# Kernel optimization log

Measured on AMD Instinct MI355X. Metric: run time of the kernel, lower is better.

## Reference

```python
import jax, jax.numpy as jnp
import numpy as np


def _topk_gate(v, k):
    # keep values >= k-th largest (ties kept, matching torch semantics)
    topk_vals = jax.lax.top_k(v, k)[0]          # (B, k)
    thr = topk_vals[:, -1:]                      # (B, 1)
    return v * (v >= thr).astype(v.dtype)


def setup_inputs() -> dict:
    key = jax.random.key(0)
    ks = jax.random.split(key, 12)
    B, S, D, R, M = 8, 2048, 1024, 64, 256
    H = 4 * D
    def lin(k, fan_out, fan_in):
        bound = 1.0 / np.sqrt(fan_in)
        return jax.random.uniform(k, (fan_out, fan_in), jnp.float32, -bound, bound)
    def bias(k, fan_out, fan_in):
        bound = 1.0 / np.sqrt(fan_in)
        return jax.random.uniform(k, (fan_out,), jnp.float32, -bound, bound)
    return {
        "x": jax.random.normal(ks[0], (B, S, D), jnp.float32),
        "state": jnp.zeros((B, M), jnp.float32),
        "U_w": lin(ks[1], R, D),
        "V_w": lin(ks[2], R, D),
        "w1": lin(ks[3], H, D),
        "b1": bias(ks[4], H, D),
        "w2": lin(ks[5], D, H),
        "b2": bias(ks[6], D, H),
        "win_w": lin(ks[7], M, D),
        "win_b": bias(ks[8], M, D),
        "wstate": lin(ks[9], M, M),
        "gamma": jnp.float32(0.9),
        "top_k": 32,
    }


def reference(x, state, U_w, V_w, w1, b1, w2, b2, win_w, win_b, wstate, gamma, top_k):
    # outputs depend only on x (residual + FFN), computed vectorized over seq.
    h = jax.nn.relu(jnp.einsum("bsd,hd->bsh", x, w1) + b1)
    outputs = x + jnp.einsum("bsh,dh->bsd", h, w2) + b2   # (B, S, D)
    # Note: U_proj / V_proj are computed but unused in the original forward
    # (dead code); omitted here as they do not affect outputs or memory.

    # precompute W_in projection for all timesteps: (B, S, M)
    x_proj = jnp.einsum("bsd,md->bsm", x, win_w) + win_b

    def step(carry, xp_t):
        st, mem = carry
        su = jax.nn.relu(st @ wstate.T + xp_t)            # (B, M)
        g = _topk_gate(su, top_k)
        mem = gamma * mem + (1.0 - gamma) * g
        return (g, mem), None

    (_, memory), _ = jax.lax.scan(step, (state, state), jnp.swapaxes(x_proj, 0, 1))
    return outputs, memory
```

## Files before the change

### kernel.cpp

```cpp
#include <hip/hip_runtime.h>
#include <stdint.h>

#define BB 8
#define SS 2048
#define DD 1024
#define HH 4096
#define MM 256

typedef short bf16x8 __attribute__((ext_vector_type(8)));
typedef float f32x4 __attribute__((ext_vector_type(4)));

__device__ inline unsigned short f2bf(float f){
  unsigned u = __builtin_bit_cast(unsigned, f);
  return (unsigned short)((u + 0x7FFFu + ((u >> 16) & 1u)) >> 16);
}

__global__ void ssma_pack_bf16(const float* __restrict__ src,
                               unsigned short* __restrict__ dst, int n4){
  int i = blockIdx.x * blockDim.x + threadIdx.x;
  if (i < n4){
    float4 v = ((const float4*)src)[i];
    ushort4 o;
    o.x = f2bf(v.x); o.y = f2bf(v.y); o.z = f2bf(v.z); o.w = f2bf(v.w);
    ((ushort4*)dst)[i] = o;
  }
}

template<int EPI>
__global__ __launch_bounds__(256) void ssma_gemm_bt(
    const unsigned short* __restrict__ A, const unsigned short* __restrict__ Bw,
    int K, int N, const float* __restrict__ bias,
    const float* __restrict__ resid, void* __restrict__ Cout)
{
  __shared__ uint4 As4[512];
  __shared__ uint4 Bs4[512];
  unsigned short* As = (unsigned short*)As4;
  unsigned short* Bs = (unsigned short*)Bs4;

  const int tid  = threadIdx.x;
  const int lane = tid & 63;
  const int wv   = tid >> 6;
  const int wm   = wv >> 1, wn = wv & 1;
  const int m0   = blockIdx.y * 128;
  const int n0   = blockIdx.x * 128;
  const int kq   = lane >> 4;
  const int rl   = lane & 15;

  f32x4 acc[4][4];
#pragma unroll
  for (int a = 0; a < 4; ++a)
#pragma unroll
    for (int b = 0; b < 4; ++b) acc[a][b] = (f32x4){0.f, 0.f, 0.f, 0.f};

  for (int k0 = 0; k0 < K; k0 += 32){
    __syncthreads();
#pragma unroll
    for (int i = 0; i < 2; ++i){
      int c  = tid + 256 * i;
      int r  = c >> 2;
      int c8 = (c & 3) * 8;
      As4[c] = *(const uint4*)(A  + (size_t)(m0 + r) * K + k0 + c8);
      Bs4[c] = *(const uint4*)(Bw + (size_t)(n0 + r) * K + k0 + c8);
    }
    __syncthreads();

    const bf16x8* Ap = (const bf16x8*)As;
    const bf16x8* Bp = (const bf16x8*)Bs;
    bf16x8 af[4], bfr[4];
#pragma unroll
    for (int mi = 0; mi < 4; ++mi) af[mi]  = Ap[(wm * 64 + mi * 16 + rl) * 4 + kq];
#pragma unroll
    for (int ni = 0; ni < 4; ++ni) bfr[ni] = Bp[(wn * 64 + ni * 16 + rl) * 4 + kq];
#pragma unroll
    for (int mi = 0; mi < 4; ++mi)
#pragma unroll
      for (int ni = 0; ni < 4; ++ni)
        acc[mi][ni] = __builtin_amdgcn_mfma_f32_16x16x32_bf16(af[mi], bfr[ni], acc[mi][ni], 0, 0, 0);
  }

#pragma unroll
  for (int mi = 0; mi < 4; ++mi){
#pragma unroll
    for (int ni = 0; ni < 4; ++ni){
      int col = n0 + wn * 64 + ni * 16 + rl;
      float bv = bias[col];
#pragma unroll
      for (int r = 0; r < 4; ++r){
        int row = m0 + wm * 64 + mi * 16 + kq * 4 + r;
        float v = acc[mi][ni][r] + bv;
        if (EPI == 0){
          v = fmaxf(v, 0.0f);
          ((unsigned short*)Cout)[(size_t)row * N + col] = f2bf(v);
        } else {
          v += resid[(size_t)row * N + col];
          ((float*)Cout)[(size_t)row * N + col] = v;
        }
      }
    }
  }
}

__global__ __launch_bounds__(256) void ssma_gemm3_f32(
    const float* __restrict__ A, const float* __restrict__ Bw,
    const float* __restrict__ bias, float* __restrict__ C)
{
  __shared__ float As[64][17];
  __shared__ float Bs[64][17];
  const int tid = threadIdx.x;
  const int tx = tid & 15, ty = tid >> 4;
  const int m0 = blockIdx.y * 64, n0 = blockIdx.x * 64;
  float acc[4][4];
#pragma unroll
  for (int i = 0; i < 4; ++i)
#pragma unroll
    for (int j = 0; j < 4; ++j) acc[i][j] = 0.f;

  for (int k0 = 0; k0 < DD; k0 += 16){
    __syncthreads();
#pragma unroll
    for (int i = 0; i < 4; ++i){
      int e = tid + 256 * i;
      int r = e >> 4, c = e & 15;
      As[r][c] = A [(size_t)(m0 + r) * DD + k0 + c];
      Bs[r][c] = Bw[(size_t)(n0 + r) * DD + k0 + c];
    }
    __syncthreads();
#pragma unroll
    for (int kk = 0; kk < 16; ++kk){
      float a[4], b[4];
#pragma unroll
      for (int i = 0; i < 4; ++i) a[i] = As[ty * 4 + i][kk];
#pragma unroll
      for (int j = 0; j < 4; ++j) b[j] = Bs[tx * 4 + j][kk];
#pragma unroll
      for (int i = 0; i < 4; ++i)
#pragma unroll
        for (int j = 0; j < 4; ++j) acc[i][j] = fmaf(a[i], b[j], acc[i][j]);
    }
  }
#pragma unroll
  for (int i = 0; i < 4; ++i){
    int row = m0 + ty * 4 + i;
#pragma unroll
    for (int j = 0; j < 4; ++j){
      int col = n0 + tx * 4 + j;
      C[(size_t)row * MM + col] = acc[i][j] + bias[col];
    }
  }
}

__global__ __launch_bounds__(256) void ssma_transpose(
    const float* __restrict__ A, float* __restrict__ At)
{
  __shared__ float t[32][33];
  const int tx = threadIdx.x & 31, ty = threadIdx.x >> 5;
  const int x0 = blockIdx.x * 32, y0 = blockIdx.y * 32;
#pragma unroll
  for (int r = 0; r < 32; r += 8)
    t[ty + r][tx] = A[(size_t)(y0 + ty + r) * MM + x0 + tx];
  __syncthreads();
#pragma unroll
  for (int r = 0; r < 32; r += 8)
    At[(size_t)(x0 + ty + r) * MM + y0 + tx] = t[tx][ty + r];
}

__global__ __launch_bounds__(1024, 4) void ssma_scan5(
    const float* __restrict__ xproj, const float* __restrict__ state,
    const float* __restrict__ wT, const float* __restrict__ gamma_p,
    const int* __restrict__ topk_p, float* __restrict__ mem_out)
{
  __shared__ __align__(16) float su_all[MM];
  __shared__ __align__(16) int   kidx[MM + 32];
  __shared__ __align__(16) float kval[MM + 32];
  __shared__ __align__(16) unsigned long long umask[4];
  __shared__ __align__(16) int   kmask16[16];

  const int tid  = threadIdx.x;
  const int wv   = tid >> 6;
  const int lane = tid & 63;
  const int b    = blockIdx.x;
  const float gamma = *gamma_p;
  const float omg   = 1.0f - gamma;
  const int   rk    = *topk_p - 1;

  const int r = tid >> 2;
  const int q = tid & 3;

  const float* xp  = xproj + (size_t)b * SS * MM;
  const float* wTm = wT + tid;

  float mem = state[b * MM + r];

  float st0 = 0.0f;
  if (tid < MM){
    st0 = state[b * MM + tid];
    unsigned long long pmi = __ballot(st0 != 0.0f);
    if (lane == 0) umask[wv] = pmi;
  }
  __syncthreads();
  int nkp;
  {
    unsigned long long u0 = umask[0], u1 = umask[1], u2 = umask[2], u3 = umask[3];
    int nk = __popcll(u0) + __popcll(u1) + __popcll(u2) + __popcll(u3);
    if (tid < MM && st0 != 0.0f){
      int before = (wv > 0 ? __popcll(u0) : 0) + (wv > 1 ? __popcll(u1) : 0)
                 + (wv > 2 ? __popcll(u2) : 0);
      unsigned long long mw = (wv == 0 ? u0 : wv == 1 ? u1 : wv == 2 ? u2 : u3);
      int pos = before + __popcll(mw & ((1ull << lane) - 1ull));
      kidx[pos] = tid << 8;
      kval[pos] = st0;
    }
    nkp = (nk + 15) & ~15; if (nkp < 32) nkp = 32;
    if (tid >= MM && tid < MM + 64){
      int t2 = tid - MM;
      if (nk + t2 < nkp){ kidx[nk + t2] = 0; kval[nk + t2] = 0.0f; }
    }
  }
  float xp_cur = (tid < MM) ? xp[tid] : 0.0f;
  __syncthreads();

  for (int t = 0; t < SS; ++t){
    float xp_next = 0.0f;
    if (tid < MM){
      int tn = (t + 1 < SS) ? t + 1 : SS - 1;
      xp_next = xp[(size_t)tn * MM + tid];

      const int4*   ip = (const int4*)kidx;
      const float4* vp = (const float4*)kval;
      int4   I[8];
      float4 V[8];
#pragma unroll
      for (int j = 0; j < 8; ++j){ I[j] = ip[j]; V[j] = vp[j]; }
      float a0=0.f,a1=0.f,a2=0.f,a3=0.f,a4=0.f,a5=0.f,a6=0.f,a7=0.f;
      float w00=wTm[I[0].x], w01=wTm[I[0].y], w02=wTm[I[0].z], w03=wTm[I[0].w];
      float w10=wTm[I[1].x], w11=wTm[I[1].y], w12=wTm[I[1].z], w13=wTm[I[1].w];
      float w20=wTm[I[2].x], w21=wTm[I[2].y], w22=wTm[I[2].z], w23=wTm[I[2].w];
      float w30=wTm[I[3].x], w31=wTm[I[3].y], w32=wTm[I[3].z], w33=wTm[I[3].w];
      float w40=wTm[I[4].x], w41=wTm[I[4].y], w42=wTm[I[4].z], w43=wTm[I[4].w];
      float w50=wTm[I[5].x], w51=wTm[I[5].y], w52=wTm[I[5].z], w53=wTm[I[5].w];
      float w60=wTm[I[6].x], w61=wTm[I[6].y], w62=wTm[I[6].z], w63=wTm[I[6].w];
      float w70=wTm[I[7].x], w71=wTm[I[7].y], w72=wTm[I[7].z], w73=wTm[I[7].w];
      a0=fmaf(w00,V[0].x,a0); a0=fmaf(w01,V[0].y,a0); a0=fmaf(w02,V[0].z,a0); a0=fmaf(w03,V[0].w,a0);
      a1=fmaf(w10,V[1].x,a1); a1=fmaf(w11,V[1].y,a1); a1=fmaf(w12,V[1].z,a1); a1=fmaf(w13,V[1].w,a1);
      a2=fmaf(w20,V[2].x,a2); a2=fmaf(w21,V[2].y,a2); a2=fmaf(w22,V[2].z,a2); a2=fmaf(w23,V[2].w,a2);
      a3=fmaf(w30,V[3].x,a3); a3=fmaf(w31,V[3].y,a3); a3=fmaf(w32,V[3].z,a3); a3=fmaf(w33,V[3].w,a3);
      a4=fmaf(w40,V[4].x,a4); a4=fmaf(w41,V[4].y,a4); a4=fmaf(w42,V[4].z,a4); a4=fmaf(w43,V[4].w,a4);
      a5=fmaf(w50,V[5].x,a5); a5=fmaf(w51,V[5].y,a5); a5=fmaf(w52,V[5].z,a5); a5=fmaf(w53,V[5].w,a5);
      a6=fmaf(w60,V[6].x,a6); a6=fmaf(w61,V[6].y,a6); a6=fmaf(w62,V[6].z,a6); a6=fmaf(w63,V[6].w,a6);
      a7=fmaf(w70,V[7].x,a7); a7=fmaf(w71,V[7].y,a7); a7=fmaf(w72,V[7].z,a7); a7=fmaf(w73,V[7].w,a7);
      if (nkp > 32){
        for (int c4 = 8; c4 < (nkp >> 2); ++c4){
          int4 I2 = ip[c4]; float4 V2 = vp[c4];
          a0 = fmaf(wTm[I2.x], V2.x, a0); a1 = fmaf(wTm[I2.y], V2.y, a1);
          a2 = fmaf(wTm[I2.z], V2.z, a2); a3 = fmaf(wTm[I2.w], V2.w, a3);
        }
      }
      float s = ((a0 + a1) + (a2 + a3)) + ((a4 + a5) + (a6 + a7));
      su_all[tid] = fmaxf(s + xp_cur, 0.0f);
    }
    __syncthreads();

    float su2 = su_all[r];
    int cnt = 0;
    const float4* spp = (const float4*)su_all;
#pragma unroll
    for (int i = 0; i < 16; ++i){
      float4 v = spp[i * 4 + q];
      cnt += (v.x > su2) + (v.y > su2) + (v.z > su2) + (v.w > su2);
    }
    cnt += __shfl_xor(cnt, 1);
    cnt += __shfl_xor(cnt, 2);

    float g = (su2 > 0.0f && cnt <= rk) ? su2 : 0.0f;
    if (q == 0) mem = fmaf(gamma, mem, omg * g);

    unsigned long long kb = __ballot(q == 0 && g > 0.0f);
    unsigned long long kbS = kb & 0x1111111111111111ull;
    if (lane == 0) kmask16[wv] = __popcll(kbS);
    __syncthreads();

    {
      int4 k0 = *(const int4*)&kmask16[0];
      int4 k1 = *(const int4*)&kmask16[4];
      int4 k2 = *(const int4*)&kmask16[8];
      int4 k3 = *(const int4*)&kmask16[12];
      int cw[16] = {k0.x,k0.y,k0.z,k0.w, k1.x,k1.y,k1.z,k1.w,
                    k2.x,k2.y,k2.z,k2.w, k3.x,k3.y,k3.z,k3.w};
      int nk = 0, before = 0;
#pragma unroll
      for (int w = 0; w < 16; ++w){
        nk += cw[w];
        if (w < wv) before += cw[w];
      }
      if (q == 0 && g > 0.0f){
        int pos = before + __popcll(kbS & ((1ull << lane) - 1ull));
        kidx[pos] = r << 8;
        kval[pos] = g;
      }
      nkp = (nk + 15) & ~15; if (nkp < 32) nkp = 32;
      if (tid < 64){
        if (nk + tid < nkp){ kidx[nk + tid] = 0; kval[nk + tid] = 0.0f; }
      }
    }
    xp_cur = xp_next;
    __syncthreads();
  }
  if (q == 0) mem_out[b * MM + r] = mem;
}

extern "C" void kernel_launch(void* const* d_in, const int* in_sizes, int n_in,
                              void* d_out, int out_size, void* d_ws, size_t ws_size,
                              hipStream_t stream)
{
  const float* x      = (const float*)d_in[0];
  const float* state  = (const float*)d_in[1];
  const float* w1     = (const float*)d_in[4];
  const float* b1     = (const float*)d_in[5];
  const float* w2     = (const float*)d_in[6];
  const float* b2     = (const float*)d_in[7];
  const float* win_w  = (const float*)d_in[8];
  const float* win_b  = (const float*)d_in[9];
  const float* wstate = (const float*)d_in[10];
  const float* gammap = (const float*)d_in[11];
  const int*   topkp  = (const int*)d_in[12];

  float* out  = (float*)d_out;
  float* memo = out + (size_t)BB * SS * DD;

  char* ws = (char*)d_ws;
  unsigned short* xb   = (unsigned short*)(ws);
  unsigned short* w1b  = (unsigned short*)(ws + 33554432);
  unsigned short* w2b  = (unsigned short*)(ws + 41943040);
  unsigned short* hbuf = (unsigned short*)(ws + 50331648);
  float*          xprj = (float*)(ws + 184549376);
  float*          wT   = (float*)(ws + 33554432);

  ssma_pack_bf16<<<16384, 256, 0, stream>>>(x,  xb,  4194304);
  ssma_pack_bf16<<<4096,  256, 0, stream>>>(w1, w1b, 1048576);
  ssma_pack_bf16<<<4096,  256, 0, stream>>>(w2, w2b, 1048576);

  ssma_gemm3_f32<<<dim3(4, 256), 256, 0, stream>>>(x, win_w, win_b, xprj);

  ssma_gemm_bt<0><<<dim3(32, 128), 256, 0, stream>>>(xb, w1b, 1024, 4096, b1, nullptr, (void*)hbuf);

  ssma_transpose<<<dim3(8, 8), 256, 0, stream>>>(wstate, wT);

  ssma_gemm_bt<1><<<dim3(8, 128), 256, 0, stream>>>(hbuf, w2b, 4096, 1024, b2, x, (void*)out);

  ssma_scan5<<<BB, 1024, 0, stream>>>(xprj, state, wT, gammap, topkp, memo);
}
```

Baseline: 5.590 ms.

## Replace rank-counting top-k in scan with exponent histogram selection

Result: slower. 6.007 ms (+7.5%).

```diff
diff --git a/kernel.cpp b/kernel.cpp
--- a/kernel.cpp
+++ b/kernel.cpp
@@ -164,16 +164,18 @@
     At[(size_t)(x0 + ty + r) * MM + y0 + tx] = t[tx][ty + r];
 }
 
-__global__ __launch_bounds__(1024, 4) void ssma_scan5(
+__global__ __launch_bounds__(1024, 4) void ssma_scan6(
     const float* __restrict__ xproj, const float* __restrict__ state,
     const float* __restrict__ wT, const float* __restrict__ gamma_p,
     const int* __restrict__ topk_p, float* __restrict__ mem_out)
 {
-  __shared__ __align__(16) float su_all[MM];
   __shared__ __align__(16) int   kidx[MM + 32];
   __shared__ __align__(16) float kval[MM + 32];
   __shared__ __align__(16) unsigned long long umask[4];
-  __shared__ __align__(16) int   kmask16[16];
+  __shared__ __align__(16) int   hist[256];
+  __shared__ __align__(16) int   suf_gt[256];
+  __shared__ __align__(16) float cand[256];
+  __shared__ int ccnt;
 
   const int tid  = threadIdx.x;
   const int wv   = tid >> 6;
@@ -181,19 +183,18 @@
   const int b    = blockIdx.x;
   const float gamma = *gamma_p;
   const float omg   = 1.0f - gamma;
-  const int   rk    = *topk_p - 1;
-
-  const int r = tid >> 2;
-  const int q = tid & 3;
+  const int   K     = *topk_p;
 
   const float* xp  = xproj + (size_t)b * SS * MM;
   const float* wTm = wT + tid;
 
-  float mem = state[b * MM + r];
-
-  float st0 = 0.0f;
+  if (tid < 64) ((int4*)hist)[tid] = (int4){0, 0, 0, 0};
+  if (tid == 1023) ccnt = 0;
+
+  float mem = 0.0f, st0 = 0.0f;
   if (tid < MM){
     st0 = state[b * MM + tid];
+    mem = st0;
     unsigned long long pmi = __ballot(st0 != 0.0f);
     if (lane == 0) umask[wv] = pmi;
   }
@@ -220,7 +221,8 @@
   __syncthreads();
 
   for (int t = 0; t < SS; ++t){
-    float xp_next = 0.0f;
+    float su = 0.0f, xp_next = 0.0f;
+    int bin = 0;
     if (tid < MM){
       int tn = (t + 1 < SS) ? t + 1 : SS - 1;
       xp_next = xp[(size_t)tn * MM + tid];
@@ -256,56 +258,81 @@
         }
       }
       float s = ((a0 + a1) + (a2 + a3)) + ((a4 + a5) + (a6 + a7));
-      su_all[tid] = fmaxf(s + xp_cur, 0.0f);
-    }
-    __syncthreads();
-
-    float su2 = su_all[r];
-    int cnt = 0;
-    const float4* spp = (const float4*)su_all;
-#pragma unroll
-    for (int i = 0; i < 16; ++i){
-      float4 v = spp[i * 4 + q];
-      cnt += (v.x > su2) + (v.y > su2) + (v.z > su2) + (v.w > su2);
-    }
-    cnt += __shfl_xor(cnt, 1);
-    cnt += __shfl_xor(cnt, 2);
-
-    float g = (su2 > 0.0f && cnt <= rk) ? su2 : 0.0f;
-    if (q == 0) mem = fmaf(gamma, mem, omg * g);
-
-    unsigned long long kb = __ballot(q == 0 && g > 0.0f);
-    unsigned long long kbS = kb & 0x1111111111111111ull;
-    if (lane == 0) kmask16[wv] = __popcll(kbS);
+      su = fmaxf(s + xp_cur, 0.0f);
+      if (su > 0.0f){
+        bin = (int)(__float_as_uint(su) >> 23);
+        atomicAdd(&hist[bin], 1);
+      }
+    }
+    __syncthreads();
+
+    if (tid < 64){
+      int4 h4 = ((const int4*)hist)[tid];
+      int t4 = h4.x + h4.y + h4.z + h4.w;
+      int I = t4;
+#pragma unroll
+      for (int off = 1; off < 64; off <<= 1){
+        int x = __shfl_down(I, off);
+        I += (lane + off < 64) ? x : 0;
+      }
+      int E = I - t4;
+      int4 s4;
+      s4.w = E;
+      s4.z = E + h4.w;
+      s4.y = s4.z + h4.z;
+      s4.x = s4.y + h4.y;
+      ((int4*)suf_gt)[tid] = s4;
+    }
+    __syncthreads();
+
+    float g = 0.0f;
+    int   a = 0;
+    bool  bound = false;
+    if (tid < MM && su > 0.0f){
+      a = suf_gt[bin];
+      int hb = hist[bin];
+      if (a >= K)            g = 0.0f;
+      else if (a + hb <= K)  g = su;
+      else { bound = true; int p = atomicAdd(&ccnt, 1); cand[p] = su; }
+    }
+    __syncthreads();
+
+    if (bound){
+      int C = __builtin_amdgcn_readfirstlane(ccnt);
+      int w = 0;
+      for (int j = 0; j < C; ++j) w += (cand[j] > su);
+      g = (a + w <= K - 1) ? su : 0.0f;
+    }
+    if (tid < MM){
+      mem = fmaf(gamma, mem, omg * g);
+      unsigned long long pm = __ballot(g > 0.0f);
+      if (lane == 0) umask[wv] = pm;
+    }
     __syncthreads();
 
     {
-      int4 k0 = *(const int4*)&kmask16[0];
-      int4 k1 = *(const int4*)&kmask16[4];
-      int4 k2 = *(const int4*)&kmask16[8];
-      int4 k3 = *(const int4*)&kmask16[12];
-      int cw[16] = {k0.x,k0.y,k0.z,k0.w, k1.x,k1.y,k1.z,k1.w,
-                    k2.x,k2.y,k2.z,k2.w, k3.x,k3.y,k3.z,k3.w};
-      int nk = 0, before = 0;
-#pragma unroll
-      for (int w = 0; w < 16; ++w){
-        nk += cw[w];
-        if (w < wv) before += cw[w];
-      }
-      if (q == 0 && g > 0.0f){
-        int pos = before + __popcll(kbS & ((1ull << lane) - 1ull));
-        kidx[pos] = r << 8;
+      unsigned long long u0 = umask[0], u1 = umask[1], u2 = umask[2], u3 = umask[3];
+      int nk = __popcll(u0) + __popcll(u1) + __popcll(u2) + __popcll(u3);
+      if (tid < MM && g > 0.0f){
+        int before = (wv > 0 ? __popcll(u0) : 0) + (wv > 1 ? __popcll(u1) : 0)
+                   + (wv > 2 ? __popcll(u2) : 0);
+        unsigned long long mw = (wv == 0 ? u0 : wv == 1 ? u1 : wv == 2 ? u2 : u3);
+        int pos = before + __popcll(mw & ((1ull << lane) - 1ull));
+        kidx[pos] = tid << 8;
         kval[pos] = g;
       }
       nkp = (nk + 15) & ~15; if (nkp < 32) nkp = 32;
-      if (tid < 64){
-        if (nk + tid < nkp){ kidx[nk + tid] = 0; kval[nk + tid] = 0.0f; }
-      }
+      if (tid >= MM && tid < MM + 64){
+        int t2 = tid - MM;
+        if (nk + t2 < nkp){ kidx[nk + t2] = 0; kval[nk + t2] = 0.0f; }
+      }
+      if (tid >= 512 && tid < 576) ((int4*)hist)[tid - 512] = (int4){0, 0, 0, 0};
+      if (tid == 1023) ccnt = 0;
     }
     xp_cur = xp_next;
     __syncthreads();
   }
-  if (q == 0) mem_out[b * MM + r] = mem;
+  if (tid < MM) mem_out[b * MM + tid] = mem;
 }
 
 extern "C" void kernel_launch(void* const* d_in, const int* in_sizes, int n_in,
@@ -347,5 +374,5 @@
 
   ssma_gemm_bt<1><<<dim3(8, 128), 256, 0, stream>>>(hbuf, w2b, 4096, 1024, b2, x, (void*)out);
 
-  ssma_scan5<<<BB, 1024, 0, stream>>>(xprj, state, wT, gammap, topkp, memo);
-}
+  ssma_scan6<<<BB, 1024, 0, stream>>>(xprj, state, wT, gammap, topkp, memo);
+}
```

## Fuse FFN GEMMs and serial scan into one persistent kernel to overlap them

Applied to the files above, without the earlier changes.

New measurement: 5.151 ms. 7.8% less time.

```diff
diff --git a/kernel.cpp b/kernel.cpp
--- a/kernel.cpp
+++ b/kernel.cpp
@@ -6,6 +6,7 @@
 #define DD 1024
 #define HH 4096
 #define MM 256
+#define NWORK 248
 
 typedef short bf16x8 __attribute__((ext_vector_type(8)));
 typedef float f32x4 __attribute__((ext_vector_type(4)));
@@ -26,67 +27,126 @@
   }
 }
 
+__global__ __launch_bounds__(256) void ssma_gemm3_f32(
+    const float* __restrict__ A, const float* __restrict__ Bw,
+    const float* __restrict__ bias, float* __restrict__ C)
+{
+  __shared__ float As[64][17];
+  __shared__ float Bs[64][17];
+  const int tid = threadIdx.x;
+  const int tx = tid & 15, ty = tid >> 4;
+  const int m0 = blockIdx.y * 64, n0 = blockIdx.x * 64;
+  float acc[4][4];
+#pragma unroll
+  for (int i = 0; i < 4; ++i)
+#pragma unroll
+    for (int j = 0; j < 4; ++j) acc[i][j] = 0.f;
+
+  for (int k0 = 0; k0 < DD; k0 += 16){
+    __syncthreads();
+#pragma unroll
+    for (int i = 0; i < 4; ++i){
+      int e = tid + 256 * i;
+      int r = e >> 4, c = e & 15;
+      As[r][c] = A [(size_t)(m0 + r) * DD + k0 + c];
+      Bs[r][c] = Bw[(size_t)(n0 + r) * DD + k0 + c];
+    }
+    __syncthreads();
+#pragma unroll
+    for (int kk = 0; kk < 16; ++kk){
+      float a[4], b[4];
+#pragma unroll
+      for (int i = 0; i < 4; ++i) a[i] = As[ty * 4 + i][kk];
+#pragma unroll
+      for (int j = 0; j < 4; ++j) b[j] = Bs[tx * 4 + j][kk];
+#pragma unroll
+      for (int i = 0; i < 4; ++i)
+#pragma unroll
+        for (int j = 0; j < 4; ++j) acc[i][j] = fmaf(a[i], b[j], acc[i][j]);
+    }
+  }
+#pragma unroll
+  for (int i = 0; i < 4; ++i){
+    int row = m0 + ty * 4 + i;
+#pragma unroll
+    for (int j = 0; j < 4; ++j){
+      int col = n0 + tx * 4 + j;
+      C[(size_t)row * MM + col] = acc[i][j] + bias[col];
+    }
+  }
+}
+
+__global__ __launch_bounds__(256) void ssma_transpose(
+    const float* __restrict__ A, float* __restrict__ At)
+{
+  __shared__ float t[32][33];
+  const int tx = threadIdx.x & 31, ty = threadIdx.x >> 5;
+  const int x0 = blockIdx.x * 32, y0 = blockIdx.y * 32;
+#pragma unroll
+  for (int r = 0; r < 32; r += 8)
+    t[ty + r][tx] = A[(size_t)(y0 + ty + r) * MM + x0 + tx];
+  __syncthreads();
+#pragma unroll
+  for (int r = 0; r < 32; r += 8)
+    At[(size_t)(x0 + ty + r) * MM + y0 + tx] = t[tx][ty + r];
+}
+
 template<int EPI>
-__global__ __launch_bounds__(256) void ssma_gemm_bt(
-    const unsigned short* __restrict__ A, const unsigned short* __restrict__ Bw,
-    int K, int N, const float* __restrict__ bias,
-    const float* __restrict__ resid, void* __restrict__ Cout)
-{
-  __shared__ uint4 As4[512];
-  __shared__ uint4 Bs4[512];
-  unsigned short* As = (unsigned short*)As4;
-  unsigned short* Bs = (unsigned short*)Bs4;
-
+__device__ void gemm_tile_1024(const unsigned short* __restrict__ A,
+                               const unsigned short* __restrict__ Bw,
+                               int K, int N, const float* __restrict__ bias,
+                               const float* __restrict__ resid, void* __restrict__ Cout,
+                               int bx, int by, uint4* As4, uint4* Bs4)
+{
   const int tid  = threadIdx.x;
   const int lane = tid & 63;
   const int wv   = tid >> 6;
-  const int wm   = wv >> 1, wn = wv & 1;
-  const int m0   = blockIdx.y * 128;
-  const int n0   = blockIdx.x * 128;
+  const int wm   = wv >> 2, wn = wv & 3;
+  const int m0   = by * 128;
+  const int n0   = bx * 128;
   const int kq   = lane >> 4;
   const int rl   = lane & 15;
 
-  f32x4 acc[4][4];
-#pragma unroll
-  for (int a = 0; a < 4; ++a)
-#pragma unroll
-    for (int b = 0; b < 4; ++b) acc[a][b] = (f32x4){0.f, 0.f, 0.f, 0.f};
+  f32x4 acc[2][2];
+#pragma unroll
+  for (int a = 0; a < 2; ++a)
+#pragma unroll
+    for (int b = 0; b < 2; ++b) acc[a][b] = (f32x4){0.f, 0.f, 0.f, 0.f};
 
   for (int k0 = 0; k0 < K; k0 += 32){
     __syncthreads();
-#pragma unroll
-    for (int i = 0; i < 2; ++i){
-      int c  = tid + 256 * i;
+    {
+      int c  = tid & 511;
       int r  = c >> 2;
       int c8 = (c & 3) * 8;
-      As4[c] = *(const uint4*)(A  + (size_t)(m0 + r) * K + k0 + c8);
-      Bs4[c] = *(const uint4*)(Bw + (size_t)(n0 + r) * K + k0 + c8);
-    }
-    __syncthreads();
-
-    const bf16x8* Ap = (const bf16x8*)As;
-    const bf16x8* Bp = (const bf16x8*)Bs;
-    bf16x8 af[4], bfr[4];
-#pragma unroll
-    for (int mi = 0; mi < 4; ++mi) af[mi]  = Ap[(wm * 64 + mi * 16 + rl) * 4 + kq];
-#pragma unroll
-    for (int ni = 0; ni < 4; ++ni) bfr[ni] = Bp[(wn * 64 + ni * 16 + rl) * 4 + kq];
-#pragma unroll
-    for (int mi = 0; mi < 4; ++mi)
-#pragma unroll
-      for (int ni = 0; ni < 4; ++ni)
+      if (tid < 512) As4[c] = *(const uint4*)(A  + (size_t)(m0 + r) * K + k0 + c8);
+      else           Bs4[c] = *(const uint4*)(Bw + (size_t)(n0 + r) * K + k0 + c8);
+    }
+    __syncthreads();
+
+    const bf16x8* Ap = (const bf16x8*)As4;
+    const bf16x8* Bp = (const bf16x8*)Bs4;
+    bf16x8 af[2], bfr[2];
+#pragma unroll
+    for (int mi = 0; mi < 2; ++mi) af[mi]  = Ap[(wm * 32 + mi * 16 + rl) * 4 + kq];
+#pragma unroll
+    for (int ni = 0; ni < 2; ++ni) bfr[ni] = Bp[(wn * 32 + ni * 16 + rl) * 4 + kq];
+#pragma unroll
+    for (int mi = 0; mi < 2; ++mi)
+#pragma unroll
+      for (int ni = 0; ni < 2; ++ni)
         acc[mi][ni] = __builtin_amdgcn_mfma_f32_16x16x32_bf16(af[mi], bfr[ni], acc[mi][ni], 0, 0, 0);
   }
 
 #pragma unroll
-  for (int mi = 0; mi < 4; ++mi){
-#pragma unroll
-    for (int ni = 0; ni < 4; ++ni){
-      int col = n0 + wn * 64 + ni * 16 + rl;
+  for (int mi = 0; mi < 2; ++mi){
+#pragma unroll
+    for (int ni = 0; ni < 2; ++ni){
+      int col = n0 + wn * 32 + ni * 16 + rl;
       float bv = bias[col];
 #pragma unroll
       for (int r = 0; r < 4; ++r){
-        int row = m0 + wm * 64 + mi * 16 + kq * 4 + r;
+        int row = m0 + wm * 32 + mi * 16 + kq * 4 + r;
         float v = acc[mi][ni][r] + bv;
         if (EPI == 0){
           v = fmaxf(v, 0.0f);
@@ -98,90 +158,65 @@
       }
     }
   }
-}
-
-__global__ __launch_bounds__(256) void ssma_gemm3_f32(
-    const float* __restrict__ A, const float* __restrict__ Bw,
-    const float* __restrict__ bias, float* __restrict__ C)
-{
-  __shared__ float As[64][17];
-  __shared__ float Bs[64][17];
-  const int tid = threadIdx.x;
-  const int tx = tid & 15, ty = tid >> 4;
-  const int m0 = blockIdx.y * 64, n0 = blockIdx.x * 64;
-  float acc[4][4];
-#pragma unroll
-  for (int i = 0; i < 4; ++i)
-#pragma unroll
-    for (int j = 0; j < 4; ++j) acc[i][j] = 0.f;
-
-  for (int k0 = 0; k0 < DD; k0 += 16){
-    __syncthreads();
-#pragma unroll
-    for (int i = 0; i < 4; ++i){
-      int e = tid + 256 * i;
-      int r = e >> 4, c = e & 15;
-      As[r][c] = A [(size_t)(m0 + r) * DD + k0 + c];
-      Bs[r][c] = Bw[(size_t)(n0 + r) * DD + k0 + c];
-    }
-    __syncthreads();
-#pragma unroll
-    for (int kk = 0; kk < 16; ++kk){
-      float a[4], b[4];
-#pragma unroll
-      for (int i = 0; i < 4; ++i) a[i] = As[ty * 4 + i][kk];
-#pragma unroll
-      for (int j = 0; j < 4; ++j) b[j] = Bs[tx * 4 + j][kk];
-#pragma unroll
-      for (int i = 0; i < 4; ++i)
-#pragma unroll
-        for (int j = 0; j < 4; ++j) acc[i][j] = fmaf(a[i], b[j], acc[i][j]);
-    }
-  }
-#pragma unroll
-  for (int i = 0; i < 4; ++i){
-    int row = m0 + ty * 4 + i;
-#pragma unroll
-    for (int j = 0; j < 4; ++j){
-      int col = n0 + tx * 4 + j;
-      C[(size_t)row * MM + col] = acc[i][j] + bias[col];
-    }
-  }
-}
-
-__global__ __launch_bounds__(256) void ssma_transpose(
-    const float* __restrict__ A, float* __restrict__ At)
-{
-  __shared__ float t[32][33];
-  const int tx = threadIdx.x & 31, ty = threadIdx.x >> 5;
-  const int x0 = blockIdx.x * 32, y0 = blockIdx.y * 32;
-#pragma unroll
-  for (int r = 0; r < 32; r += 8)
-    t[ty + r][tx] = A[(size_t)(y0 + ty + r) * MM + x0 + tx];
-  __syncthreads();
-#pragma unroll
-  for (int r = 0; r < 32; r += 8)
-    At[(size_t)(x0 + ty + r) * MM + y0 + tx] = t[tx][ty + r];
-}
-
-__global__ __launch_bounds__(1024, 4) void ssma_scan5(
+  __syncthreads();
+}
+
+__global__ __launch_bounds__(1024, 1) void ssma_fused2(
     const float* __restrict__ xproj, const float* __restrict__ state,
     const float* __restrict__ wT, const float* __restrict__ gamma_p,
-    const int* __restrict__ topk_p, float* __restrict__ mem_out)
-{
+    const int* __restrict__ topk_p, float* __restrict__ mem_out,
+    const unsigned short* __restrict__ xb, const unsigned short* __restrict__ w1b,
+    const unsigned short* __restrict__ w2b, unsigned short* __restrict__ hbuf,
+    const float* __restrict__ b1, const float* __restrict__ b2,
+    const float* __restrict__ xres, float* __restrict__ out,
+    unsigned int* __restrict__ ctr)
+{
+  __shared__ uint4 As4[512];
+  __shared__ uint4 Bs4[512];
   __shared__ __align__(16) float su_all[MM];
   __shared__ __align__(16) int   kidx[MM + 32];
   __shared__ __align__(16) float kval[MM + 32];
   __shared__ __align__(16) unsigned long long umask[4];
   __shared__ __align__(16) int   kmask16[16];
-
-  const int tid  = threadIdx.x;
+  __shared__ char pad_[66000];
+
+  const int tid = threadIdx.x;
+  const int K   = *topk_p;
+  if (K == -987654) pad_[0] = (char)K;
+
+  unsigned int* done = ctr + 1;
+
+  if (blockIdx.x >= 8){
+    const int wid = blockIdx.x - 8;
+    for (int t = wid; t < 4096; t += NWORK)
+      gemm_tile_1024<0>(xb, w1b, 1024, 4096, b1, nullptr, (void*)hbuf, t & 31, t >> 5, As4, Bs4);
+    if (tid == 0){
+      __threadfence();
+      atomicAdd(ctr, 1u);
+      while (__hip_atomic_load(ctr, __ATOMIC_RELAXED, __HIP_MEMORY_SCOPE_AGENT) < NWORK)
+        __builtin_amdgcn_s_sleep(16);
+    }
+    __syncthreads();
+    __threadfence();
+    for (int t = wid; t < 1024; t += NWORK)
+      gemm_tile_1024<1>(hbuf, w2b, 4096, 1024, b2, xres, (void*)out, t & 7, t >> 3, As4, Bs4);
+
+    float dummy = 1.0f + (float)tid * 1e-7f;
+    while (__hip_atomic_load(done, __ATOMIC_RELAXED, __HIP_MEMORY_SCOPE_AGENT) < 8u){
+#pragma unroll
+      for (int i = 0; i < 64; ++i) dummy = fmaf(dummy, 1.0000001f, 1e-9f);
+      asm volatile("" :: "v"(dummy));
+      __builtin_amdgcn_s_sleep(2);
+    }
+    return;
+  }
+
+  const int b    = blockIdx.x;
   const int wv   = tid >> 6;
   const int lane = tid & 63;
-  const int b    = blockIdx.x;
   const float gamma = *gamma_p;
   const float omg   = 1.0f - gamma;
-  const int   rk    = *topk_p - 1;
+  const int   rk    = K - 1;
 
   const int r = tid >> 2;
   const int q = tid & 3;
@@ -306,6 +341,11 @@
     __syncthreads();
   }
   if (q == 0) mem_out[b * MM + r] = mem;
+  __syncthreads();
+  if (tid == 0){
+    __threadfence();
+    atomicAdd(done, 1u);
+  }
 }
 
 extern "C" void kernel_launch(void* const* d_in, const int* in_sizes, int n_in,
@@ -333,19 +373,19 @@
   unsigned short* w2b  = (unsigned short*)(ws + 41943040);
   unsigned short* hbuf = (unsigned short*)(ws + 50331648);
   float*          xprj = (float*)(ws + 184549376);
-  float*          wT   = (float*)(ws + 33554432);
+  float*          wT   = (float*)(ws + 201326592);
+  unsigned int*   ctr  = (unsigned int*)(ws + 201326592 + 262144);
 
   ssma_pack_bf16<<<16384, 256, 0, stream>>>(x,  xb,  4194304);
   ssma_pack_bf16<<<4096,  256, 0, stream>>>(w1, w1b, 1048576);
   ssma_pack_bf16<<<4096,  256, 0, stream>>>(w2, w2b, 1048576);
 
   ssma_gemm3_f32<<<dim3(4, 256), 256, 0, stream>>>(x, win_w, win_b, xprj);
-
-  ssma_gemm_bt<0><<<dim3(32, 128), 256, 0, stream>>>(xb, w1b, 1024, 4096, b1, nullptr, (void*)hbuf);
-
   ssma_transpose<<<dim3(8, 8), 256, 0, stream>>>(wstate, wT);
 
-  ssma_gemm_bt<1><<<dim3(8, 128), 256, 0, stream>>>(hbuf, w2b, 4096, 1024, b2, x, (void*)out);
-
-  ssma_scan5<<<BB, 1024, 0, stream>>>(xprj, state, wT, gammap, topkp, memo);
-}
+  hipMemsetAsync(ctr, 0, 8, stream);
+
+  ssma_fused2<<<8 + NWORK, 1024, 0, stream>>>(
+      xprj, state, wT, gammap, topkp, memo,
+      xb, w1b, w2b, hbuf, b1, b2, x, out, ctr);
+}
```
